# Kernel tuning notes

Measured on AMD Instinct MI355X. Metric: run time of the kernel, lower is better.

## Reference

```python
import math
import jax, jax.numpy as jnp
import numpy as np

H = 16  # num_heads
B, L, D = 1, 256, 1024


def setup_inputs() -> dict:
    key = jax.random.key(0)
    ks = jax.random.split(key, 12)
    s = 1.0 / math.sqrt(D)  # keep activations O(1)
    inp = {
        "mu": jax.random.normal(ks[0], (B, L, D), jnp.float32),
        "var": jax.random.uniform(ks[1], (B, L, D), jnp.float32) + 0.1,
    }
    names = ["q_mu", "q_var", "k_mu", "k_var", "v_mu", "v_var", "o_mu", "o_var"]
    for i, n in enumerate(names):
        inp["w" + n] = jax.random.normal(ks[2 + i], (D, D), jnp.float32) * s
        inp["b" + n] = jnp.zeros((D,), jnp.float32)
    return inp


def _split_heads(x):
    b, l, d = x.shape
    return x.reshape(b, l, H, d // H).transpose(0, 2, 1, 3)  # [B,H,L,Dh]


def _combine_heads(x):
    b, h, l, dh = x.shape
    return x.transpose(0, 2, 1, 3).reshape(b, l, h * dh)


def reference(mu, var, wq_mu, bq_mu, wq_var, bq_var, wk_mu, bk_mu, wk_var, bk_var,
              wv_mu, bv_mu, wv_var, bv_var, wo_mu, bo_mu, wo_var, bo_var):
    dk = mu.shape[-1] // H
    Qm = _split_heads(mu @ wq_mu + bq_mu)
    Qv = _split_heads(jax.nn.softplus(var @ wq_var + bq_var))
    Km = _split_heads(mu @ wk_mu + bk_mu)
    Kv = _split_heads(jax.nn.softplus(var @ wk_var + bk_var))
    Vm = _split_heads(mu @ wv_mu + bv_mu)
    Vv = _split_heads(jax.nn.softplus(var @ wv_var + bv_var))

    # per-element Gaussian KL, broadcast to [B,H,Lq,Lk,Dh] (as in the original)
    diff = (Qm[:, :, :, None, :] - Km[:, :, None, :, :]) ** 2
    ratio = Qv[:, :, :, None, :] / Kv[:, :, None, :, :]
    kl = diff / (2.0 * Kv[:, :, None, :, :]) + 0.5 * (ratio - jnp.log(ratio) - 1.0)
    scores = -kl.sum(-1) * (1.0 / math.sqrt(dk))  # [B,H,Lq,Lk]
    attn = jax.nn.softmax(scores, axis=-1)

    out_mu = jnp.einsum("bhqk,bhkd->bhqd", attn, Vm)
    out_var = jnp.einsum("bhqk,bhkd->bhqd", attn ** 2, Vv)

    O_mu = _combine_heads(out_mu)
    O_var = _combine_heads(out_var)
    mu_out = O_mu @ wo_mu + bo_mu
    var_out = jax.nn.softplus(O_var @ wo_var + bo_var)
    return mu_out, var_out
```

## Files before the change

### kernel.cpp

```cpp
#include <hip/hip_runtime.h>
#include <math.h>

typedef __bf16 bf16_t;
typedef bf16_t bf16x4 __attribute__((ext_vector_type(4)));
typedef bf16_t bf16x8 __attribute__((ext_vector_type(8)));
typedef float  f32x4  __attribute__((ext_vector_type(4)));

__device__ __forceinline__ float softplus_f(float x) {
    return (x > 20.f) ? x : log1pf(expf(x));
}

__device__ __forceinline__ float fast_rcp(float x) {
#if __has_builtin(__builtin_amdgcn_rcpf)
    return __builtin_amdgcn_rcpf(x);
#else
    return 1.0f / x;
#endif
}

struct PrepArgs { const float* src[8]; const float* mu; const float* var; };

__global__ __launch_bounds__(256) void prep_kernel(PrepArgs pa, bf16_t* __restrict__ wtbase,
                                                   bf16_t* __restrict__ dmu, bf16_t* __restrict__ dvar) {
    const int t = threadIdx.x;
    if (blockIdx.z == 8) {
        const int gid = (blockIdx.y * 16 + blockIdx.x) * 256 + t;
        const float* s; bf16_t* d; int off;
        if (gid < 32768) { s = pa.mu;  d = dmu;  off = gid * 8; }
        else             { s = pa.var; d = dvar; off = (gid - 32768) * 8; }
        float4 v0 = *(const float4*)(s + off);
        float4 v1 = *(const float4*)(s + off + 4);
        bf16x8 o;
        o[0] = (bf16_t)v0.x; o[1] = (bf16_t)v0.y; o[2] = (bf16_t)v0.z; o[3] = (bf16_t)v0.w;
        o[4] = (bf16_t)v1.x; o[5] = (bf16_t)v1.y; o[6] = (bf16_t)v1.z; o[7] = (bf16_t)v1.w;
        *(bf16x8*)(d + off) = o;
        return;
    }
    const int kt = blockIdx.x, nt = blockIdx.y, wm = blockIdx.z;
    const float* __restrict__ W = pa.src[wm];
    bf16_t* __restrict__ Wt = wtbase + (size_t)wm * 1048576;
    __shared__ bf16_t Ts[64][72];
    const int r0 = t >> 4, c4 = (t & 15) * 4;
#pragma unroll
    for (int rep = 0; rep < 4; ++rep) {
        const int r = r0 + rep * 16;
        const float4 v = *(const float4*)&W[(size_t)(kt * 64 + r) * 1024 + nt * 64 + c4];
        Ts[c4 + 0][r] = (bf16_t)v.x;
        Ts[c4 + 1][r] = (bf16_t)v.y;
        Ts[c4 + 2][r] = (bf16_t)v.z;
        Ts[c4 + 3][r] = (bf16_t)v.w;
    }
    __syncthreads();
#pragma unroll
    for (int rep = 0; rep < 2; ++rep) {
        const int chunk = t + rep * 256;
        const int n = chunk >> 3, kc = (chunk & 7) * 8;
        bf16x8 v = *(const bf16x8*)&Ts[n][kc];
        *(bf16x8*)&Wt[(size_t)(nt * 64 + n) * 1024 + kt * 64 + kc] = v;
    }
}

struct GemmArgs {
    const bf16_t* A[6];
    const bf16_t* Wt[6];
    const float*  bias[6];
    float*        dst[6];
    int           splus[6];
};

__global__ __launch_bounds__(256, 2) void gemm_splitk(GemmArgs args) {
    const int z = blockIdx.z;
    const bf16_t* __restrict__ A    = args.A[z];
    const bf16_t* __restrict__ Wt   = args.Wt[z];
    const float*  __restrict__ bias = args.bias[z];
    float*        __restrict__ dst  = args.dst[z];
    const int sp = args.splus[z];

    const int n_base = blockIdx.x * 64;
    const int m_base = blockIdx.y * 64;

    __shared__ __align__(16) unsigned char smem_raw[73728];
    bf16_t* stage = (bf16_t*)smem_raw;
    float*  Cr    = (float*)smem_raw;

    const int t = threadIdx.x;
    const int lane = t & 63;
    const int w = t >> 6;
    bf16_t* As = stage + w * 9216;
    bf16_t* Bs = As + 4608;

    const int r8 = lane >> 3, kb = lane & 7;
    const int fr = lane & 15, fq = lane >> 4, fk = fq * 8;

    f32x4 acc[4][4] = {};

#pragma unroll
    for (int s = 0; s < 4; ++s) {
        const int k0 = w * 256 + s * 64;
#pragma unroll
        for (int i = 0; i < 8; ++i) {
            const int row = i * 8 + r8;
            bf16x8 av = *(const bf16x8*)&A [(size_t)(m_base + row) * 1024 + k0 + kb * 8];
            bf16x8 bv = *(const bf16x8*)&Wt[(size_t)(n_base + row) * 1024 + k0 + kb * 8];
            *(bf16x8*)&As[row * 72 + kb * 8] = av;
            *(bf16x8*)&Bs[row * 72 + kb * 8] = bv;
        }
#pragma unroll
        for (int kh = 0; kh < 2; ++kh) {
            bf16x8 aF[4], bF[4];
#pragma unroll
            for (int i = 0; i < 4; ++i)
                aF[i] = *(const bf16x8*)&As[(i * 16 + fr) * 72 + kh * 32 + fk];
#pragma unroll
            for (int j = 0; j < 4; ++j)
                bF[j] = *(const bf16x8*)&Bs[(j * 16 + fr) * 72 + kh * 32 + fk];
#pragma unroll
            for (int i = 0; i < 4; ++i)
#pragma unroll
                for (int j = 0; j < 4; ++j)
                    acc[i][j] = __builtin_amdgcn_mfma_f32_16x16x32_bf16(aF[i], bF[j], acc[i][j], 0, 0, 0);
        }
    }

    __syncthreads();
    {
        float* Crw = Cr + w * 4352;
        const int orow = fq * 4;
#pragma unroll
        for (int i = 0; i < 4; ++i)
#pragma unroll
            for (int j = 0; j < 4; ++j)
#pragma unroll
                for (int rr = 0; rr < 4; ++rr)
                    Crw[(i * 16 + orow + rr) * 68 + j * 16 + fr] = acc[i][j][rr];
    }
    __syncthreads();

    const int cc = (t & 15) * 4;
    f32x4 bv4 = *(const f32x4*)&bias[n_base + cc];
#pragma unroll
    for (int i = 0; i < 4; ++i) {
        const int row = (t >> 4) + i * 16;
        f32x4 s0 = *(const f32x4*)&Cr[0 * 4352 + row * 68 + cc];
        f32x4 s1 = *(const f32x4*)&Cr[1 * 4352 + row * 68 + cc];
        f32x4 s2 = *(const f32x4*)&Cr[2 * 4352 + row * 68 + cc];
        f32x4 s3 = *(const f32x4*)&Cr[3 * 4352 + row * 68 + cc];
        f32x4 v = (s0 + s1) + (s2 + s3) + bv4;
        if (sp) {
            v[0] = softplus_f(v[0]); v[1] = softplus_f(v[1]);
            v[2] = softplus_f(v[2]); v[3] = softplus_f(v[3]);
        }
        *(f32x4*)&dst[(size_t)(m_base + row) * 1024 + n_base + cc] = v;
    }
}

__global__ __launch_bounds__(256) void feat_kernel(const float* __restrict__ Km,
                                                   const float* __restrict__ Kv,
                                                   float* __restrict__ G,
                                                   float* __restrict__ cvec) {
    const int h = blockIdx.x, kb = blockIdx.y;
    const int t = threadIdx.x;
    const int kx = t & 63;
    const int dg = t >> 6;
    const int k = kb * 64 + kx;
    const float* kvp = Kv + (size_t)k * 1024 + h * 64 + dg * 16;
    const float* kmp = Km + (size_t)k * 1024 + h * 64 + dg * 16;
    float* gbase = G + (size_t)h * 32768;
    float cp = 0.f;
#pragma unroll
    for (int c = 0; c < 4; ++c) {
        f32x4 kv = *(const f32x4*)(kvp + c * 4);
        f32x4 km = *(const f32x4*)(kmp + c * 4);
#pragma unroll
        for (int e = 0; e < 4; ++e) {
            const int d = dg * 16 + c * 4 + e;
            const float r = 0.5f * fast_rcp(kv[e]);
            gbase[(size_t)d * 256 + k]        = r;
            gbase[(size_t)(64 + d) * 256 + k] = -2.f * km[e] * r;
            cp += km[e] * km[e] * r + 0.5f * __logf(kv[e]);
        }
    }
    __shared__ float red[4][64];
    red[dg][kx] = cp;
    __syncthreads();
    if (dg == 0)
        cvec[h * 256 + k] = red[0][kx] + red[1][kx] + red[2][kx] + red[3][kx];
}

#define OFF_VM   0
#define OFF_VV   36864
#define OFF_GS   73728
#define OFF_FS   90368
#define OFF_PHI  73728
#define OFF_PLO  82176
#define OFF_P2HI 90624
#define OFF_P2LO 99072
#define ATTN_SMEM 107520

__global__ __launch_bounds__(256) void attn_v5(const float* __restrict__ Qm,
                                               const float* __restrict__ Qv,
                                               const float* __restrict__ G,
                                               const float* __restrict__ cvec,
                                               const float* __restrict__ Vm,
                                               const float* __restrict__ Vv,
                                               bf16_t* __restrict__ Omu,
                                               bf16_t* __restrict__ Ovar) {
    __shared__ __align__(16) unsigned char smem[ATTN_SMEM];
    bf16_t* Vsm = (bf16_t*)(smem + OFF_VM);
    bf16_t* Vsv = (bf16_t*)(smem + OFF_VV);
    float*  Gs  = (float*)(smem + OFF_GS);
    float*  Fs  = (float*)(smem + OFF_FS);
    bf16_t* Phi = (bf16_t*)(smem + OFF_PHI);
    bf16_t* Plo = (bf16_t*)(smem + OFF_PLO);
    bf16_t* P2h = (bf16_t*)(smem + OFF_P2HI);
    bf16_t* P2l = (bf16_t*)(smem + OFF_P2LO);

    const int qt = blockIdx.x, h = blockIdx.y;
    const int t = threadIdx.x, w = t >> 6, lane = t & 63;
    const int fr = lane & 15, fq = lane >> 4;
    const int fw = w * 4;

    {
        const int r = t >> 4, c = t & 15;
        f32x4 qm = *(const f32x4*)(Qm + (size_t)(qt * 16 + r) * 1024 + h * 64 + c * 4);
        f32x4 qv = *(const f32x4*)(Qv + (size_t)(qt * 16 + r) * 1024 + h * 64 + c * 4);
        *(f32x4*)&Fs[r * 132 + c * 4]      = qm * qm + qv;
        *(f32x4*)&Fs[r * 132 + 64 + c * 4] = qm;
    }

    const float* gsrc = G + (size_t)h * 32768 + (size_t)(t >> 4) * 256 + (t & 15) * 16;
    {
        f32x4 g0 = *(const f32x4*)(gsrc);
        f32x4 g1 = *(const f32x4*)(gsrc + 4);
        f32x4 g2 = *(const f32x4*)(gsrc + 8);
        f32x4 g3 = *(const f32x4*)(gsrc + 12);
        float* gd = &Gs[(t >> 4) * 260 + (t & 15) * 16];
        *(f32x4*)(gd)      = g0;
        *(f32x4*)(gd + 4)  = g1;
        *(f32x4*)(gd + 8)  = g2;
        *(f32x4*)(gd + 12) = g3;
    }
    __syncthreads();

    f32x4 acc0 = {0.f,0.f,0.f,0.f}, acc1 = acc0, acc2 = acc0, acc3 = acc0;
    const int vk = t >> 2, vpart = t & 3;

    for (int c = 0; c < 8; ++c) {
        f32x4 g0, g1, g2, g3;
        if (c < 7) {
            const float* s = gsrc + (size_t)(c + 1) * 4096;
            g0 = *(const f32x4*)(s);
            g1 = *(const f32x4*)(s + 4);
            g2 = *(const f32x4*)(s + 8);
            g3 = *(const f32x4*)(s + 12);
        }
        const int rep = c & 3;
        const int kkv = vk + rep * 64;
        const float* vsrc = ((c >> 2) ? Vv : Vm) + (size_t)kkv * 1024 + h * 64 + vpart * 16;
        f32x4 v0 = *(const f32x4*)(vsrc);
        f32x4 v1 = *(const f32x4*)(vsrc + 4);
        f32x4 v2 = *(const f32x4*)(vsrc + 8);
        f32x4 v3 = *(const f32x4*)(vsrc + 12);

#pragma unroll
        for (int dl = 0; dl < 16; ++dl) {
            f32x4 g = *(const f32x4*)&Gs[dl * 260 + lane * 4];
            const int d = c * 16 + dl;
            acc0 += Fs[(fw + 0) * 132 + d] * g;
            acc1 += Fs[(fw + 1) * 132 + d] * g;
            acc2 += Fs[(fw + 2) * 132 + d] * g;
            acc3 += Fs[(fw + 3) * 132 + d] * g;
        }
        __syncthreads();
        {
            bf16_t* vdst = ((c >> 2) ? Vsv : Vsm) + kkv * 72 + vpart * 16;
            bf16x8 o0, o1;
            o0[0]=(bf16_t)v0[0]; o0[1]=(bf16_t)v0[1]; o0[2]=(bf16_t)v0[2]; o0[3]=(bf16_t)v0[3];
            o0[4]=(bf16_t)v1[0]; o0[5]=(bf16_t)v1[1]; o0[6]=(bf16_t)v1[2]; o0[7]=(bf16_t)v1[3];
            o1[0]=(bf16_t)v2[0]; o1[1]=(bf16_t)v2[1]; o1[2]=(bf16_t)v2[2]; o1[3]=(bf16_t)v2[3];
            o1[4]=(bf16_t)v3[0]; o1[5]=(bf16_t)v3[1]; o1[6]=(bf16_t)v3[2]; o1[7]=(bf16_t)v3[3];
            *(bf16x8*)(vdst)     = o0;
            *(bf16x8*)(vdst + 8) = o1;
        }
        if (c < 7) {
            float* gd = &Gs[(t >> 4) * 260 + (t & 15) * 16];
            *(f32x4*)(gd)      = g0;
            *(f32x4*)(gd + 4)  = g1;
            *(f32x4*)(gd + 8)  = g2;
            *(f32x4*)(gd + 12) = g3;
        }
        __syncthreads();
    }

    const f32x4 c4 = *(const f32x4*)&cvec[h * 256 + lane * 4];
    f32x4 sr[4];
    sr[0] = (acc0 + c4) * (-0.125f);
    sr[1] = (acc1 + c4) * (-0.125f);
    sr[2] = (acc2 + c4) * (-0.125f);
    sr[3] = (acc3 + c4) * (-0.125f);

#pragma unroll
    for (int r = 0; r < 4; ++r) {
        f32x4 s = sr[r];
        float mloc = fmaxf(fmaxf(s[0], s[1]), fmaxf(s[2], s[3]));
#pragma unroll
        for (int off = 32; off > 0; off >>= 1)
            mloc = fmaxf(mloc, __shfl_xor(mloc, off, 64));
        s[0] = __expf(s[0] - mloc); s[1] = __expf(s[1] - mloc);
        s[2] = __expf(s[2] - mloc); s[3] = __expf(s[3] - mloc);
        float sl = (s[0] + s[1]) + (s[2] + s[3]);
#pragma unroll
        for (int off = 32; off > 0; off >>= 1)
            sl += __shfl_xor(sl, off, 64);
        sr[r] = s * fast_rcp(sl);
    }

#pragma unroll
    for (int r = 0; r < 4; ++r) {
        bf16x4 phi, plo, p2hi, p2lo;
#pragma unroll
        for (int e = 0; e < 4; ++e) {
            const float p = sr[r][e];
            const bf16_t hb = (bf16_t)p;
            phi[e] = hb; plo[e] = (bf16_t)(p - (float)hb);
            const float p2 = p * p;
            const bf16_t h2 = (bf16_t)p2;
            p2hi[e] = h2; p2lo[e] = (bf16_t)(p2 - (float)h2);
        }
        const int row = fw + r;
        *(bf16x4*)&Phi[row * 264 + lane * 4] = phi;
        *(bf16x4*)&Plo[row * 264 + lane * 4] = plo;
        *(bf16x4*)&P2h[row * 264 + lane * 4] = p2hi;
        *(bf16x4*)&P2l[row * 264 + lane * 4] = p2lo;
    }
    __syncthreads();

    f32x4 accm = {0.f,0.f,0.f,0.f}, accv = {0.f,0.f,0.f,0.f};
#pragma unroll
    for (int k0 = 0; k0 < 256; k0 += 32) {
        const int ka = k0 + fq * 8;
        bf16x8 ahi = *(const bf16x8*)&Phi[fr * 264 + ka];
        bf16x8 alo = *(const bf16x8*)&Plo[fr * 264 + ka];
        bf16x8 a2h = *(const bf16x8*)&P2h[fr * 264 + ka];
        bf16x8 a2l = *(const bf16x8*)&P2l[fr * 264 + ka];
        bf16x8 bm, bv;
#pragma unroll
        for (int j = 0; j < 8; ++j) {
            const int kk = ka + j;
            bm[j] = Vsm[kk * 72 + w * 16 + fr];
            bv[j] = Vsv[kk * 72 + w * 16 + fr];
        }
        accm = __builtin_amdgcn_mfma_f32_16x16x32_bf16(ahi, bm, accm, 0, 0, 0);
        accm = __builtin_amdgcn_mfma_f32_16x16x32_bf16(alo, bm, accm, 0, 0, 0);
        accv = __builtin_amdgcn_mfma_f32_16x16x32_bf16(a2h, bv, accv, 0, 0, 0);
        accv = __builtin_amdgcn_mfma_f32_16x16x32_bf16(a2l, bv, accv, 0, 0, 0);
    }

#pragma unroll
    for (int reg = 0; reg < 4; ++reg) {
        const int qg = qt * 16 + fq * 4 + reg;
        const size_t ob = (size_t)qg * 1024 + h * 64 + w * 16 + fr;
        Omu[ob]  = (bf16_t)accm[reg];
        Ovar[ob] = (bf16_t)accv[reg];
    }
}

extern "C" void kernel_launch(void* const* d_in, const int* in_sizes, int n_in,
                              void* d_out, int out_size, void* d_ws, size_t ws_size,
                              hipStream_t stream) {
    const float* mu  = (const float*)d_in[0];
    const float* var = (const float*)d_in[1];

    uint8_t* ws = (uint8_t*)d_ws;
    bf16_t* Abf_mu  = (bf16_t*)(ws);
    bf16_t* Abf_var = (bf16_t*)(ws + (512u << 10));
    bf16_t* WtB     = (bf16_t*)(ws + (1u << 20));
    float*  Proj    = (float*)(ws + (17u << 20));
    bf16_t* Obf_mu  = (bf16_t*)(ws + (23u << 20));
    bf16_t* Obf_var = (bf16_t*)(ws + (23u << 20) + (512u << 10));
    float*  G       = (float*)(ws + (24u << 20));
    float*  cvec    = (float*)(ws + (26u << 20));

    PrepArgs pa;
    for (int i = 0; i < 8; ++i) pa.src[i] = (const float*)d_in[2 + 2 * i];
    pa.mu = mu; pa.var = var;
    prep_kernel<<<dim3(16, 16, 9), 256, 0, stream>>>(pa, WtB, Abf_mu, Abf_var);

    GemmArgs g1;
    for (int z = 0; z < 6; ++z) {
        g1.A[z]    = (z & 1) ? Abf_var : Abf_mu;
        g1.Wt[z]   = WtB + (size_t)z * 1048576;
        g1.bias[z] = (const float*)d_in[3 + 2 * z];
        g1.dst[z]  = Proj + (size_t)z * 262144;
        g1.splus[z] = (z & 1);
    }
    gemm_splitk<<<dim3(16, 4, 6), 256, 0, stream>>>(g1);

    feat_kernel<<<dim3(16, 4), 256, 0, stream>>>(Proj + 2 * 262144, Proj + 3 * 262144, G, cvec);

    attn_v5<<<dim3(16, 16), 256, 0, stream>>>(Proj,
                                              Proj + 262144,
                                              G, cvec,
                                              Proj + 4 * 262144,
                                              Proj + 5 * 262144,
                                              Obf_mu, Obf_var);

    GemmArgs g3;
    for (int z = 0; z < 6; ++z) {
        g3.A[z]    = Obf_mu;
        g3.Wt[z]   = WtB + (size_t)6 * 1048576;
        g3.bias[z] = (const float*)d_in[15];
        g3.dst[z]  = (float*)d_out;
        g3.splus[z] = 0;
    }
    g3.A[1]    = Obf_var;
    g3.Wt[1]   = WtB + (size_t)7 * 1048576;
    g3.bias[1] = (const float*)d_in[17];
    g3.dst[1]  = (float*)d_out + 262144;
    g3.splus[1] = 1;
    gemm_splitk<<<dim3(16, 4, 2), 256, 0, stream>>>(g3);
}
```

Before: 153.0 us.

## Compute KL attention scores with bf16 MFMA using split-precision query features

The score computation (query features times per-key G matrix) moves from scalar FP32 FMA over shared-memory-staged G tiles to MFMA bf16 instructions. The query features are split into hi/lo bf16 parts to keep accuracy. G is now written by the feature kernel as a bf16 row-major [h, k, 128] layout and read directly from global into registers with prefetch, which removes the G shared-memory staging loop and its per-chunk barriers. Scores pass through a new shared-memory buffer before the softmax. G itself is only bf16, which adds rounding error to the KL scores, and the kernel uses more shared memory.

```diff
diff --git a/kernel.cpp b/kernel.cpp
--- a/kernel.cpp
+++ b/kernel.cpp
@@ -156,50 +156,52 @@
 
 __global__ __launch_bounds__(256) void feat_kernel(const float* __restrict__ Km,
                                                    const float* __restrict__ Kv,
-                                                   float* __restrict__ G,
+                                                   bf16_t* __restrict__ Gbf,
                                                    float* __restrict__ cvec) {
     const int h = blockIdx.x, kb = blockIdx.y;
     const int t = threadIdx.x;
     const int kx = t & 63;
     const int dg = t >> 6;
-    const int k = kb * 64 + kx;
-    const float* kvp = Kv + (size_t)k * 1024 + h * 64 + dg * 16;
-    const float* kmp = Km + (size_t)k * 1024 + h * 64 + dg * 16;
-    float* gbase = G + (size_t)h * 32768;
+    const int katt = kb * 64 + kx;
+    const float* kvp = Kv + (size_t)katt * 1024 + h * 64 + dg * 16;
+    const float* kmp = Km + (size_t)katt * 1024 + h * 64 + dg * 16;
+    bf16_t* grow = Gbf + ((size_t)(h * 256 + katt)) * 128;
     float cp = 0.f;
 #pragma unroll
     for (int c = 0; c < 4; ++c) {
         f32x4 kv = *(const f32x4*)(kvp + c * 4);
         f32x4 km = *(const f32x4*)(kmp + c * 4);
+        bf16x4 o1, o2;
 #pragma unroll
         for (int e = 0; e < 4; ++e) {
-            const int d = dg * 16 + c * 4 + e;
             const float r = 0.5f * fast_rcp(kv[e]);
-            gbase[(size_t)d * 256 + k]        = r;
-            gbase[(size_t)(64 + d) * 256 + k] = -2.f * km[e] * r;
+            o1[e] = (bf16_t)r;
+            o2[e] = (bf16_t)(-2.f * km[e] * r);
             cp += km[e] * km[e] * r + 0.5f * __logf(kv[e]);
         }
+        *(bf16x4*)&grow[dg * 16 + c * 4]      = o1;
+        *(bf16x4*)&grow[64 + dg * 16 + c * 4] = o2;
     }
     __shared__ float red[4][64];
     red[dg][kx] = cp;
     __syncthreads();
     if (dg == 0)
-        cvec[h * 256 + k] = red[0][kx] + red[1][kx] + red[2][kx] + red[3][kx];
+        cvec[h * 256 + katt] = red[0][kx] + red[1][kx] + red[2][kx] + red[3][kx];
 }
 
 #define OFF_VM   0
 #define OFF_VV   36864
-#define OFF_GS   73728
-#define OFF_FS   90368
-#define OFF_PHI  73728
-#define OFF_PLO  82176
-#define OFF_P2HI 90624
-#define OFF_P2LO 99072
-#define ATTN_SMEM 107520
-
-__global__ __launch_bounds__(256) void attn_v5(const float* __restrict__ Qm,
+#define OFF_FS   73728
+#define OFF_SC   82176
+#define OFF_PHI  98816
+#define OFF_PLO  107264
+#define OFF_P2H  115712
+#define OFF_P2L  124160
+#define ATTN_SMEM 132608
+
+__global__ __launch_bounds__(256) void attn_v6(const float* __restrict__ Qm,
                                                const float* __restrict__ Qv,
-                                               const float* __restrict__ G,
+                                               const bf16_t* __restrict__ Gbf,
                                                const float* __restrict__ cvec,
                                                const float* __restrict__ Vm,
                                                const float* __restrict__ Vv,
@@ -208,17 +210,23 @@
     __shared__ __align__(16) unsigned char smem[ATTN_SMEM];
     bf16_t* Vsm = (bf16_t*)(smem + OFF_VM);
     bf16_t* Vsv = (bf16_t*)(smem + OFF_VV);
-    float*  Gs  = (float*)(smem + OFF_GS);
     float*  Fs  = (float*)(smem + OFF_FS);
+    float*  Sc  = (float*)(smem + OFF_SC);
     bf16_t* Phi = (bf16_t*)(smem + OFF_PHI);
     bf16_t* Plo = (bf16_t*)(smem + OFF_PLO);
-    bf16_t* P2h = (bf16_t*)(smem + OFF_P2HI);
-    bf16_t* P2l = (bf16_t*)(smem + OFF_P2LO);
+    bf16_t* P2h = (bf16_t*)(smem + OFF_P2H);
+    bf16_t* P2l = (bf16_t*)(smem + OFF_P2L);
 
     const int qt = blockIdx.x, h = blockIdx.y;
     const int t = threadIdx.x, w = t >> 6, lane = t & 63;
     const int fr = lane & 15, fq = lane >> 4;
-    const int fw = w * 4;
+    const int n0 = w * 64;
+
+    const bf16_t* gB = Gbf + ((size_t)(h * 256 + n0 + fr)) * 128 + fq * 8;
+
+    bf16x8 bcur[4];
+#pragma unroll
+    for (int ks = 0; ks < 4; ++ks) bcur[ks] = *(const bf16x8*)(gB + ks * 32);
 
     {
         const int r = t >> 4, c = t & 15;
@@ -227,78 +235,81 @@
         *(f32x4*)&Fs[r * 132 + c * 4]      = qm * qm + qv;
         *(f32x4*)&Fs[r * 132 + 64 + c * 4] = qm;
     }
-
-    const float* gsrc = G + (size_t)h * 32768 + (size_t)(t >> 4) * 256 + (t & 15) * 16;
-    {
-        f32x4 g0 = *(const f32x4*)(gsrc);
-        f32x4 g1 = *(const f32x4*)(gsrc + 4);
-        f32x4 g2 = *(const f32x4*)(gsrc + 8);
-        f32x4 g3 = *(const f32x4*)(gsrc + 12);
-        float* gd = &Gs[(t >> 4) * 260 + (t & 15) * 16];
-        *(f32x4*)(gd)      = g0;
-        *(f32x4*)(gd + 4)  = g1;
-        *(f32x4*)(gd + 8)  = g2;
-        *(f32x4*)(gd + 12) = g3;
-    }
-    __syncthreads();
-
-    f32x4 acc0 = {0.f,0.f,0.f,0.f}, acc1 = acc0, acc2 = acc0, acc3 = acc0;
+    __syncthreads();
+
+    bf16x8 ahi[4], alo[4];
+#pragma unroll
+    for (int ks = 0; ks < 4; ++ks) {
+        f32x4 f0 = *(const f32x4*)&Fs[fr * 132 + ks * 32 + fq * 8];
+        f32x4 f1 = *(const f32x4*)&Fs[fr * 132 + ks * 32 + fq * 8 + 4];
+#pragma unroll
+        for (int e = 0; e < 4; ++e) {
+            bf16_t hb = (bf16_t)f0[e];
+            ahi[ks][e] = hb; alo[ks][e] = (bf16_t)(f0[e] - (float)hb);
+            bf16_t hb2 = (bf16_t)f1[e];
+            ahi[ks][e + 4] = hb2; alo[ks][e + 4] = (bf16_t)(f1[e] - (float)hb2);
+        }
+    }
+
     const int vk = t >> 2, vpart = t & 3;
-
-    for (int c = 0; c < 8; ++c) {
-        f32x4 g0, g1, g2, g3;
-        if (c < 7) {
-            const float* s = gsrc + (size_t)(c + 1) * 4096;
-            g0 = *(const f32x4*)(s);
-            g1 = *(const f32x4*)(s + 4);
-            g2 = *(const f32x4*)(s + 8);
-            g3 = *(const f32x4*)(s + 12);
-        }
-        const int rep = c & 3;
-        const int kkv = vk + rep * 64;
-        const float* vsrc = ((c >> 2) ? Vv : Vm) + (size_t)kkv * 1024 + h * 64 + vpart * 16;
-        f32x4 v0 = *(const f32x4*)(vsrc);
-        f32x4 v1 = *(const f32x4*)(vsrc + 4);
-        f32x4 v2 = *(const f32x4*)(vsrc + 8);
-        f32x4 v3 = *(const f32x4*)(vsrc + 12);
-
-#pragma unroll
-        for (int dl = 0; dl < 16; ++dl) {
-            f32x4 g = *(const f32x4*)&Gs[dl * 260 + lane * 4];
-            const int d = c * 16 + dl;
-            acc0 += Fs[(fw + 0) * 132 + d] * g;
-            acc1 += Fs[(fw + 1) * 132 + d] * g;
-            acc2 += Fs[(fw + 2) * 132 + d] * g;
-            acc3 += Fs[(fw + 3) * 132 + d] * g;
-        }
-        __syncthreads();
+#pragma unroll
+    for (int nt = 0; nt < 4; ++nt) {
+        const int ua = 2 * nt, ub = 2 * nt + 1;
+        const float* vsa = ((ua >> 2) ? Vv : Vm) + (size_t)(vk + (ua & 3) * 64) * 1024 + h * 64 + vpart * 16;
+        const float* vsb = ((ub >> 2) ? Vv : Vm) + (size_t)(vk + (ub & 3) * 64) * 1024 + h * 64 + vpart * 16;
+        f32x4 va0 = *(const f32x4*)(vsa),     va1 = *(const f32x4*)(vsa + 4);
+        f32x4 va2 = *(const f32x4*)(vsa + 8), va3 = *(const f32x4*)(vsa + 12);
+        f32x4 vb0 = *(const f32x4*)(vsb),     vb1 = *(const f32x4*)(vsb + 4);
+        f32x4 vb2 = *(const f32x4*)(vsb + 8), vb3 = *(const f32x4*)(vsb + 12);
+
+        bf16x8 bnxt[4];
+        if (nt < 3) {
+#pragma unroll
+            for (int ks = 0; ks < 4; ++ks)
+                bnxt[ks] = *(const bf16x8*)(gB + (size_t)(nt + 1) * 2048 + ks * 32);
+        }
+
+        f32x4 acc = {0.f, 0.f, 0.f, 0.f};
+#pragma unroll
+        for (int ks = 0; ks < 4; ++ks) {
+            acc = __builtin_amdgcn_mfma_f32_16x16x32_bf16(ahi[ks], bcur[ks], acc, 0, 0, 0);
+            acc = __builtin_amdgcn_mfma_f32_16x16x32_bf16(alo[ks], bcur[ks], acc, 0, 0, 0);
+        }
+
         {
-            bf16_t* vdst = ((c >> 2) ? Vsv : Vsm) + kkv * 72 + vpart * 16;
+            bf16_t* da = ((ua >> 2) ? Vsv : Vsm) + (vk + (ua & 3) * 64) * 72 + vpart * 16;
+            bf16_t* db = ((ub >> 2) ? Vsv : Vsm) + (vk + (ub & 3) * 64) * 72 + vpart * 16;
             bf16x8 o0, o1;
-            o0[0]=(bf16_t)v0[0]; o0[1]=(bf16_t)v0[1]; o0[2]=(bf16_t)v0[2]; o0[3]=(bf16_t)v0[3];
-            o0[4]=(bf16_t)v1[0]; o0[5]=(bf16_t)v1[1]; o0[6]=(bf16_t)v1[2]; o0[7]=(bf16_t)v1[3];
-            o1[0]=(bf16_t)v2[0]; o1[1]=(bf16_t)v2[1]; o1[2]=(bf16_t)v2[2]; o1[3]=(bf16_t)v2[3];
-            o1[4]=(bf16_t)v3[0]; o1[5]=(bf16_t)v3[1]; o1[6]=(bf16_t)v3[2]; o1[7]=(bf16_t)v3[3];
-            *(bf16x8*)(vdst)     = o0;
-            *(bf16x8*)(vdst + 8) = o1;
-        }
-        if (c < 7) {
-            float* gd = &Gs[(t >> 4) * 260 + (t & 15) * 16];
-            *(f32x4*)(gd)      = g0;
-            *(f32x4*)(gd + 4)  = g1;
-            *(f32x4*)(gd + 8)  = g2;
-            *(f32x4*)(gd + 12) = g3;
-        }
-        __syncthreads();
-    }
-
-    const f32x4 c4 = *(const f32x4*)&cvec[h * 256 + lane * 4];
+            o0[0]=(bf16_t)va0[0]; o0[1]=(bf16_t)va0[1]; o0[2]=(bf16_t)va0[2]; o0[3]=(bf16_t)va0[3];
+            o0[4]=(bf16_t)va1[0]; o0[5]=(bf16_t)va1[1]; o0[6]=(bf16_t)va1[2]; o0[7]=(bf16_t)va1[3];
+            o1[0]=(bf16_t)va2[0]; o1[1]=(bf16_t)va2[1]; o1[2]=(bf16_t)va2[2]; o1[3]=(bf16_t)va2[3];
+            o1[4]=(bf16_t)va3[0]; o1[5]=(bf16_t)va3[1]; o1[6]=(bf16_t)va3[2]; o1[7]=(bf16_t)va3[3];
+            *(bf16x8*)(da)     = o0;
+            *(bf16x8*)(da + 8) = o1;
+            o0[0]=(bf16_t)vb0[0]; o0[1]=(bf16_t)vb0[1]; o0[2]=(bf16_t)vb0[2]; o0[3]=(bf16_t)vb0[3];
+            o0[4]=(bf16_t)vb1[0]; o0[5]=(bf16_t)vb1[1]; o0[6]=(bf16_t)vb1[2]; o0[7]=(bf16_t)vb1[3];
+            o1[0]=(bf16_t)vb2[0]; o1[1]=(bf16_t)vb2[1]; o1[2]=(bf16_t)vb2[2]; o1[3]=(bf16_t)vb2[3];
+            o1[4]=(bf16_t)vb3[0]; o1[5]=(bf16_t)vb3[1]; o1[6]=(bf16_t)vb3[2]; o1[7]=(bf16_t)vb3[3];
+            *(bf16x8*)(db)     = o0;
+            *(bf16x8*)(db + 8) = o1;
+        }
+
+        const float cv = cvec[h * 256 + n0 + nt * 16 + fr];
+        f32x4 lg = (acc + cv) * (-0.125f);
+#pragma unroll
+        for (int reg = 0; reg < 4; ++reg)
+            Sc[(fq * 4 + reg) * 260 + n0 + nt * 16 + fr] = lg[reg];
+
+#pragma unroll
+        for (int ks = 0; ks < 4; ++ks) bcur[ks] = bnxt[ks];
+    }
+    __syncthreads();
+
+    const int fw = w * 4;
     f32x4 sr[4];
-    sr[0] = (acc0 + c4) * (-0.125f);
-    sr[1] = (acc1 + c4) * (-0.125f);
-    sr[2] = (acc2 + c4) * (-0.125f);
-    sr[3] = (acc3 + c4) * (-0.125f);
-
+#pragma unroll
+    for (int r = 0; r < 4; ++r)
+        sr[r] = *(const f32x4*)&Sc[(fw + r) * 260 + lane * 4];
 #pragma unroll
     for (int r = 0; r < 4; ++r) {
         f32x4 s = sr[r];
@@ -339,10 +350,10 @@
 #pragma unroll
     for (int k0 = 0; k0 < 256; k0 += 32) {
         const int ka = k0 + fq * 8;
-        bf16x8 ahi = *(const bf16x8*)&Phi[fr * 264 + ka];
-        bf16x8 alo = *(const bf16x8*)&Plo[fr * 264 + ka];
-        bf16x8 a2h = *(const bf16x8*)&P2h[fr * 264 + ka];
-        bf16x8 a2l = *(const bf16x8*)&P2l[fr * 264 + ka];
+        bf16x8 ahi2 = *(const bf16x8*)&Phi[fr * 264 + ka];
+        bf16x8 alo2 = *(const bf16x8*)&Plo[fr * 264 + ka];
+        bf16x8 a2h  = *(const bf16x8*)&P2h[fr * 264 + ka];
+        bf16x8 a2l  = *(const bf16x8*)&P2l[fr * 264 + ka];
         bf16x8 bm, bv;
 #pragma unroll
         for (int j = 0; j < 8; ++j) {
@@ -350,10 +361,10 @@
             bm[j] = Vsm[kk * 72 + w * 16 + fr];
             bv[j] = Vsv[kk * 72 + w * 16 + fr];
         }
-        accm = __builtin_amdgcn_mfma_f32_16x16x32_bf16(ahi, bm, accm, 0, 0, 0);
-        accm = __builtin_amdgcn_mfma_f32_16x16x32_bf16(alo, bm, accm, 0, 0, 0);
-        accv = __builtin_amdgcn_mfma_f32_16x16x32_bf16(a2h, bv, accv, 0, 0, 0);
-        accv = __builtin_amdgcn_mfma_f32_16x16x32_bf16(a2l, bv, accv, 0, 0, 0);
+        accm = __builtin_amdgcn_mfma_f32_16x16x32_bf16(ahi2, bm, accm, 0, 0, 0);
+        accm = __builtin_amdgcn_mfma_f32_16x16x32_bf16(alo2, bm, accm, 0, 0, 0);
+        accv = __builtin_amdgcn_mfma_f32_16x16x32_bf16(a2h,  bv, accv, 0, 0, 0);
+        accv = __builtin_amdgcn_mfma_f32_16x16x32_bf16(a2l,  bv, accv, 0, 0, 0);
     }
 
 #pragma unroll
@@ -378,8 +389,8 @@
     float*  Proj    = (float*)(ws + (17u << 20));
     bf16_t* Obf_mu  = (bf16_t*)(ws + (23u << 20));
     bf16_t* Obf_var = (bf16_t*)(ws + (23u << 20) + (512u << 10));
-    float*  G       = (float*)(ws + (24u << 20));
-    float*  cvec    = (float*)(ws + (26u << 20));
+    bf16_t* Gbf     = (bf16_t*)(ws + (24u << 20));
+    float*  cvec    = (float*)(ws + (25u << 20));
 
     PrepArgs pa;
     for (int i = 0; i < 8; ++i) pa.src[i] = (const float*)d_in[2 + 2 * i];
@@ -396,11 +407,11 @@
     }
     gemm_splitk<<<dim3(16, 4, 6), 256, 0, stream>>>(g1);
 
-    feat_kernel<<<dim3(16, 4), 256, 0, stream>>>(Proj + 2 * 262144, Proj + 3 * 262144, G, cvec);
-
-    attn_v5<<<dim3(16, 16), 256, 0, stream>>>(Proj,
+    feat_kernel<<<dim3(16, 4), 256, 0, stream>>>(Proj + 2 * 262144, Proj + 3 * 262144, Gbf, cvec);
+
+    attn_v6<<<dim3(16, 16), 256, 0, stream>>>(Proj,
                                               Proj + 262144,
-                                              G, cvec,
+                                              Gbf, cvec,
                                               Proj + 4 * 262144,
                                               Proj + 5 * 262144,
                                               Obf_mu, Obf_var);
```

Result: no change. 150.6 us, median of 2 (-1.6%).
